# Kernel tuning notes

Measured on AMD Instinct MI355X. Metric: run time of the kernel, lower is better.

The kernel has to match this reference:

```python
import jax, jax.numpy as jnp
import numpy as np

NUM_HEADS = 16

def setup_inputs() -> dict:
    key = jax.random.key(0)
    ks = jax.random.split(key, 10)
    B, S, D = 2, 2048, 1024
    q = jax.random.normal(ks[0], (B, S, D), dtype=jnp.float32)
    k = jax.random.normal(ks[1], (B, S, D), dtype=jnp.float32)
    v = jax.random.normal(ks[2], (B, S, D), dtype=jnp.float32)
    mask = jax.random.randint(ks[3], (B, S), 0, 2, dtype=jnp.int32)
    scale = 0.02
    Wq = jax.random.normal(ks[4], (D, D), dtype=jnp.float32) * scale
    bq = jax.random.normal(ks[5], (D,), dtype=jnp.float32) * scale
    Wk = jax.random.normal(ks[6], (D, D), dtype=jnp.float32) * scale
    bk = jax.random.normal(ks[7], (D,), dtype=jnp.float32) * scale
    Wv = jax.random.normal(ks[8], (D, D), dtype=jnp.float32) * scale
    bv = jax.random.normal(ks[9], (D,), dtype=jnp.float32) * scale
    return {"q": q, "k": k, "v": v, "mask": mask,
            "Wq": Wq, "bq": bq, "Wk": Wk, "bk": bk, "Wv": Wv, "bv": bv}


def reference(q, k, v, mask, Wq, bq, Wk, bk, Wv, bv):
    B, S, D = q.shape
    H = NUM_HEADS
    dh = D // H
    # per-head split along last dim == reshape to (B, S, H, dh)
    Qh = (q @ Wq + bq).reshape(B, S, H, dh)
    Kh = (k @ Wk + bk).reshape(B, S, H, dh)
    Vh = (v @ Wv + bv).reshape(B, S, H, dh)
    # NOTE: original scales by sqrt(10), not sqrt(dim_per_head)
    scores = jnp.einsum('bqhd,bkhd->bhqk', Qh, Kh) / jnp.sqrt(jnp.float32(10.0))
    # mask [B,S] masks key positions; masked_fill replaces with -1e9
    scores = jnp.where(mask[:, None, None, :] == 0, jnp.float32(-1e9), scores)
    probs = jax.nn.softmax(scores, axis=-1)
    out = jnp.einsum('bhqk,bkhd->bqhd', probs, Vh).reshape(B, S, D)
    return out
```

## Files before the change

### kernel.cpp

```cpp
#include <hip/hip_runtime.h>
#include <hip/hip_bf16.h>

typedef __attribute__((ext_vector_type(8))) short short8;
typedef __attribute__((ext_vector_type(4))) float f32x4;

#define SC_L2E 0.4561727848849353f

#if __has_builtin(__builtin_amdgcn_exp2f)
#define EXP2F __builtin_amdgcn_exp2f
#else
#define EXP2F exp2f
#endif

static __device__ __forceinline__ void gload16(const void* g, void* l) {
  __builtin_amdgcn_global_load_lds((const __attribute__((address_space(1))) void*)g,
                                   (__attribute__((address_space(3))) void*)l, 16, 0, 0);
}

__global__ void k_cvt(const float* __restrict__ q, const float* __restrict__ kk,
                      const float* __restrict__ v, __hip_bfloat16* __restrict__ xb,
                      const float* __restrict__ Wq, const float* __restrict__ Wk,
                      const float* __restrict__ Wv, __hip_bfloat16* __restrict__ wt,
                      const int* __restrict__ mask, float* __restrict__ bias2) {
  __shared__ float T[64][65];
  if (blockIdx.x < 6144) {
    const size_t i = ((size_t)blockIdx.x * 256 + threadIdx.x) * 8;
    const int t = (int)(i >> 22);
    const float* src = (t == 0) ? q : (t == 1) ? kk : v;
    const size_t off = i & 4194303u;
    float4 f0 = *(const float4*)(src + off);
    float4 f1 = *(const float4*)(src + off + 4);
    union { short8 s; __hip_bfloat16 h[8]; } u;
    u.h[0] = __float2bfloat16(f0.x); u.h[1] = __float2bfloat16(f0.y);
    u.h[2] = __float2bfloat16(f0.z); u.h[3] = __float2bfloat16(f0.w);
    u.h[4] = __float2bfloat16(f1.x); u.h[5] = __float2bfloat16(f1.y);
    u.h[6] = __float2bfloat16(f1.z); u.h[7] = __float2bfloat16(f1.w);
    *(short8*)((char*)xb + i * 2) = u.s;
    return;
  }
  const int idx2 = blockIdx.x - 6144;
  const int z = idx2 >> 8;
  const int r2 = idx2 & 255;
  const int bxi = r2 & 15, byi = r2 >> 4;
  if (z == 0 && byi == 0) {
    const int idx = bxi * 256 + threadIdx.x;
    bias2[idx] = mask[idx] ? -12.0f : -1e30f;
  }
  const float* W = (z == 0) ? Wq : (z == 1) ? Wk : Wv;
  __hip_bfloat16* Wd = wt + (size_t)z * 1048576;
  const int n0 = bxi * 64, k0 = byi * 64;
  const int tx = threadIdx.x & 63, ty = threadIdx.x >> 6;
#pragma unroll
  for (int r = 0; r < 16; ++r)
    T[ty + r * 4][tx] = W[(size_t)(k0 + ty + r * 4) * 1024 + n0 + tx];
  __syncthreads();
#pragma unroll
  for (int r = 0; r < 16; ++r)
    Wd[(size_t)(n0 + ty + r * 4) * 1024 + k0 + tx] = __float2bfloat16(T[tx][ty + r * 4]);
}

__global__ __launch_bounds__(256) void k_proj(
    const __hip_bfloat16* __restrict__ xb, const __hip_bfloat16* __restrict__ wt,
    const float* __restrict__ bq, const float* __restrict__ bk, const float* __restrict__ bv,
    __hip_bfloat16* __restrict__ Qb, __hip_bfloat16* __restrict__ Kb,
    __hip_bfloat16* __restrict__ Vt) {
  __shared__ char smem[32768];
  char* As = smem;
  char* Bs = smem + 16384;
  const int orig = blockIdx.x;
  const int xcd = orig & 7, idx = orig >> 3;
  const int by = xcd * 4 + (idx & 3);
  const int bx = (idx >> 2) & 7;
  const int t = idx >> 5;
  const char* X = (const char*)(xb + (size_t)t * 4194304);
  const char* W = (const char*)(wt + (size_t)t * 1048576);
  const float* bias = (t == 0) ? bq : (t == 1) ? bk : bv;
  const int m0 = by * 128, n0 = bx * 128;
  const int tid = threadIdx.x, w = tid >> 6, lane = tid & 63;
  const int l15 = lane & 15, g = lane >> 4;
  const int l8 = lane >> 3, l7 = lane & 7;
  const int vswz = ((l7 ^ l8) << 4);
  const int wm = (w >> 1) * 64, wn = (w & 1) * 64;
  f32x4 acc[4][4];
#pragma unroll
  for (int i = 0; i < 4; ++i)
#pragma unroll
    for (int j = 0; j < 4; ++j) acc[i][j] = (f32x4){0.f, 0.f, 0.f, 0.f};

  for (int k0 = 0; k0 < 2048; k0 += 128) {
    __syncthreads();
#pragma unroll
    for (int j = 0; j < 4; ++j) {
      const int ch = w * 4 + j;
      gload16(X + (size_t)(m0 + ch * 8 + l8) * 2048 + k0 + vswz, As + ch * 1024);
      gload16(W + (size_t)(n0 + ch * 8 + l8) * 2048 + k0 + vswz, Bs + ch * 1024);
    }
    __syncthreads();
#pragma unroll
    for (int kk = 0; kk < 2; ++kk) {
      short8 af[4], bf_[4];
#pragma unroll
      for (int mt = 0; mt < 4; ++mt) {
        const int row = wm + mt * 16 + l15;
        af[mt] = *(const short8*)(As + row * 128 + ((kk * 64 + g * 16) ^ ((row & 7) << 4)));
      }
#pragma unroll
      for (int nt = 0; nt < 4; ++nt) {
        const int row = wn + nt * 16 + l15;
        bf_[nt] = *(const short8*)(Bs + row * 128 + ((kk * 64 + g * 16) ^ ((row & 7) << 4)));
      }
#pragma unroll
      for (int mt = 0; mt < 4; ++mt)
#pragma unroll
        for (int nt = 0; nt < 4; ++nt)
          acc[mt][nt] = __builtin_amdgcn_mfma_f32_16x16x32_bf16(af[mt], bf_[nt], acc[mt][nt], 0, 0, 0);
    }
  }

  float bv4[4];
#pragma unroll
  for (int nt = 0; nt < 4; ++nt) bv4[nt] = bias[n0 + wn + nt * 16 + l15];

  if (t < 2) {
#pragma unroll
    for (int mt = 0; mt < 4; ++mt) {
#pragma unroll
      for (int nt = 0; nt < 4; ++nt) {
        const int feat = n0 + wn + nt * 16 + l15;
        const int h = feat >> 6, d = feat & 63;
#pragma unroll
        for (int r = 0; r < 4; ++r) {
          const int token = m0 + wm + mt * 16 + g * 4 + r;
          const int b = token >> 11, s = token & 2047;
          const float val = acc[mt][nt][r] + bv4[nt];
          const __hip_bfloat16 hb = __float2bfloat16(val);
          if (t == 0) Qb[((size_t)(b * 16 + h) * 2048 + s) * 64 + d] = hb;
          else        Kb[((size_t)(b * 16 + h) * 2048 + s) * 64 + d] = hb;
        }
      }
    }
  } else {
    __hip_bfloat16* T2 = (__hip_bfloat16*)smem;
    const int bb = m0 >> 11;
    const int s0 = m0 & 2047;
#pragma unroll
    for (int p = 0; p < 2; ++p) {
      __syncthreads();
      if ((w >> 1) == p) {
#pragma unroll
        for (int mt = 0; mt < 4; ++mt)
#pragma unroll
          for (int nt = 0; nt < 4; ++nt) {
            const int feat = wn + nt * 16 + l15;
#pragma unroll
            for (int r = 0; r < 4; ++r) {
              const int tok = mt * 16 + g * 4 + r;
              T2[feat * 64 + (tok ^ ((feat & 7) << 3))] =
                  __float2bfloat16(acc[mt][nt][r] + bv4[nt]);
            }
          }
      }
      __syncthreads();
#pragma unroll
      for (int sw = 0; sw < 4; ++sw) {
        const int row = sw * 32 + (tid >> 3);
        const int c = tid & 7;
        const short8 vchunk = *(const short8*)(smem + row * 128 + 16 * (c ^ (row & 7)));
        const int gfeat = n0 + row;
        const int hh = gfeat >> 6, dd = gfeat & 63;
        *(short8*)(Vt + ((size_t)((bb * 16 + hh) * 64 + dd)) * 2048 + s0 + p * 64 + c * 8) = vchunk;
      }
    }
  }
}

#define ATTN_BODY(CUR, PRF, PREF)                                              \
  {                                                                            \
    float4 mb[4];                                                              \
    _Pragma("unroll") for (int nt = 0; nt < 4; ++nt)                           \
        mb[nt] = *(const float4*)(mbp + (nt >> 1) * 32 + ((nt & 1) << 2) + g * 8); \
    mbp += 64;                                                                 \
    if (PREF) {                                                                \
      gload16(kst, Ks[PRF] + w * 1024);                                        \
      gload16(vst, Vs[PRF] + w * 1024);                                        \
    }                                                                          \
    kst += 8192; vst += 128;                                                   \
    f32x4 s_[4];                                                               \
    __builtin_amdgcn_s_setprio(1);                                             \
    _Pragma("unroll") for (int nt = 0; nt < 4; ++nt) {                         \
      s_[nt] = (f32x4){0.f, 0.f, 0.f, 0.f};                                    \
      const int key = nt * 16 + l15;                                           \
      _Pragma("unroll") for (int kc = 0; kc < 2; ++kc) {                       \
        const short8 kf = *(const short8*)(Ks[CUR] + key * 128 +               \
                           ((kc * 64 + g * 16) ^ ((key & 7) << 4)));           \
        s_[nt] = __builtin_amdgcn_mfma_f32_16x16x32_bf16(kf, aq[kc], s_[nt], 0, 0, 0); \
      }                                                                        \
    }                                                                          \
    __builtin_amdgcn_s_setprio(0);                                             \
    short8 pb8[2];                                                             \
    _Pragma("unroll") for (int c = 0; c < 2; ++c) {                            \
      union { short8 s8; __hip_bfloat16 hh[8]; } pu;                           \
      pu.hh[0] = __float2bfloat16(EXP2F(fmaf(s_[2*c][0], SC_L2E, mb[2*c].x))); \
      pu.hh[1] = __float2bfloat16(EXP2F(fmaf(s_[2*c][1], SC_L2E, mb[2*c].y))); \
      pu.hh[2] = __float2bfloat16(EXP2F(fmaf(s_[2*c][2], SC_L2E, mb[2*c].z))); \
      pu.hh[3] = __float2bfloat16(EXP2F(fmaf(s_[2*c][3], SC_L2E, mb[2*c].w))); \
      pu.hh[4] = __float2bfloat16(EXP2F(fmaf(s_[2*c+1][0], SC_L2E, mb[2*c+1].x))); \
      pu.hh[5] = __float2bfloat16(EXP2F(fmaf(s_[2*c+1][1], SC_L2E, mb[2*c+1].y))); \
      pu.hh[6] = __float2bfloat16(EXP2F(fmaf(s_[2*c+1][2], SC_L2E, mb[2*c+1].z))); \
      pu.hh[7] = __float2bfloat16(EXP2F(fmaf(s_[2*c+1][3], SC_L2E, mb[2*c+1].w))); \
      pb8[c] = pu.s8;                                                          \
    }                                                                          \
    __builtin_amdgcn_s_setprio(1);                                             \
    lacc = __builtin_amdgcn_mfma_f32_16x16x32_bf16(ones8, pb8[0], lacc, 0, 0, 0); \
    lacc = __builtin_amdgcn_mfma_f32_16x16x32_bf16(ones8, pb8[1], lacc, 0, 0, 0); \
    _Pragma("unroll") for (int dt = 0; dt < 4; ++dt) {                         \
      const int d = dt * 16 + l15;                                             \
      const int sw2 = (d & 7) << 4;                                            \
      f32x4 o = oaccT[dt];                                                     \
      const short8 v0 = *(const short8*)(Vs[CUR] + d * 128 + ((g * 16) ^ sw2)); \
      const short8 v1 = *(const short8*)(Vs[CUR] + d * 128 + ((64 + g * 16) ^ sw2)); \
      o = __builtin_amdgcn_mfma_f32_16x16x32_bf16(v0, pb8[0], o, 0, 0, 0);     \
      o = __builtin_amdgcn_mfma_f32_16x16x32_bf16(v1, pb8[1], o, 0, 0, 0);     \
      oaccT[dt] = o;                                                           \
    }                                                                          \
    __builtin_amdgcn_s_setprio(0);                                             \
    asm volatile("s_waitcnt vmcnt(2)" ::: "memory");                           \
    __builtin_amdgcn_s_barrier();                                              \
    __builtin_amdgcn_sched_barrier(0);                                         \
  }

__global__ __launch_bounds__(512, 2) void k_attn(
    const __hip_bfloat16* __restrict__ Qb, const __hip_bfloat16* __restrict__ Kb,
    const __hip_bfloat16* __restrict__ Vt, const float* __restrict__ bias2,
    float* __restrict__ out) {
  __shared__ char Ks[3][8192];
  __shared__ char Vs[3][8192];
  const int orig = blockIdx.x;
  const int swz = (orig & 7) * 64 + (orig >> 3);
  const int bh = swz >> 4, qb = swz & 15;
  const int b = bh >> 4, h = bh & 15;
  const int tid = threadIdx.x, w = tid >> 6, lane = tid & 63;
  const int g = lane >> 4, l15 = lane & 15;
  const char* Qc = (const char*)(Qb + (size_t)bh * 131072);
  const char* Kc = (const char*)(Kb + (size_t)bh * 131072);
  const char* Vc = (const char*)(Vt + (size_t)bh * 131072);

  const int l8 = lane >> 3, l7 = lane & 7;
  const int vswz = ((l7 ^ l8) << 4);

  short8 aq[2];
  const int arow = qb * 128 + w * 16 + l15;
#pragma unroll
  for (int kc = 0; kc < 2; ++kc)
    aq[kc] = *(const short8*)(Qc + (size_t)arow * 128 + kc * 64 + g * 16);

  f32x4 oaccT[4];
#pragma unroll
  for (int i = 0; i < 4; ++i) oaccT[i] = (f32x4){0.f, 0.f, 0.f, 0.f};
  f32x4 lacc = (f32x4){0.f, 0.f, 0.f, 0.f};
  const short8 ones8 = {(short)0x3F80, (short)0x3F80, (short)0x3F80, (short)0x3F80,
                        (short)0x3F80, (short)0x3F80, (short)0x3F80, (short)0x3F80};

  const int s = w * 8 + l8;
  const int nt0 = s >> 4, gg = (s >> 2) & 3, rr = s & 3;
  const int kap = (nt0 >> 1) * 32 + gg * 8 + ((nt0 & 1) << 2) + rr;
  const char* kst = Kc + (size_t)kap * 128 + vswz;
  const char* vst = Vc + (size_t)s * 4096 + vswz;
  gload16(kst, Ks[0] + w * 1024);
  gload16(vst, Vs[0] + w * 1024);
  kst += 8192; vst += 128;
  gload16(kst, Ks[1] + w * 1024);
  gload16(vst, Vs[1] + w * 1024);
  kst += 8192; vst += 128;
  asm volatile("s_waitcnt vmcnt(2)" ::: "memory");
  __builtin_amdgcn_s_barrier();
  __builtin_amdgcn_sched_barrier(0);

  const float* mbp = bias2 + b * 2048;
  for (int kt = 0; kt < 30; kt += 3) {
    ATTN_BODY(0, 2, true)
    ATTN_BODY(1, 0, true)
    ATTN_BODY(2, 1, true)
  }
  ATTN_BODY(0, 2, false)
  ATTN_BODY(1, 0, false)

  const float rl = 1.0f / lacc[0];
  float* orow = out + ((size_t)(b * 2048 + arow)) * 1024 + h * 64;
#pragma unroll
  for (int dt = 0; dt < 4; ++dt) {
    float4 st;
    st.x = oaccT[dt][0] * rl; st.y = oaccT[dt][1] * rl;
    st.z = oaccT[dt][2] * rl; st.w = oaccT[dt][3] * rl;
    *(float4*)(orow + dt * 16 + g * 4) = st;
  }
}

extern "C" void kernel_launch(void* const* d_in, const int* in_sizes, int n_in,
                              void* d_out, int out_size, void* d_ws, size_t ws_size,
                              hipStream_t stream) {
  const float* q   = (const float*)d_in[0];
  const float* k   = (const float*)d_in[1];
  const float* v   = (const float*)d_in[2];
  const int* mask  = (const int*)d_in[3];
  const float* Wq  = (const float*)d_in[4];
  const float* bq  = (const float*)d_in[5];
  const float* Wk  = (const float*)d_in[6];
  const float* bk  = (const float*)d_in[7];
  const float* Wv  = (const float*)d_in[8];
  const float* bv  = (const float*)d_in[9];
  float* out = (float*)d_out;
  char* ws = (char*)d_ws;
  __hip_bfloat16* Xb = (__hip_bfloat16*)(ws);
  __hip_bfloat16* Wt = (__hip_bfloat16*)(ws + 25165824);
  __hip_bfloat16* Qb = (__hip_bfloat16*)(ws + 31457280);
  __hip_bfloat16* Kb = (__hip_bfloat16*)(ws + 39845888);
  __hip_bfloat16* Vt = (__hip_bfloat16*)(ws + 48234496);
  float* bias2      = (float*)(ws + 56623104);

  k_cvt<<<dim3(6912), dim3(256), 0, stream>>>(q, k, v, Xb, Wq, Wk, Wv, Wt, mask, bias2);
  k_proj<<<dim3(768), dim3(256), 0, stream>>>(Xb, Wt, bq, bk, bv, Qb, Kb, Vt);
  k_attn<<<dim3(512), dim3(512), 0, stream>>>(Qb, Kb, Vt, bias2, out);
}
```

Measured before the change: 103.9 us.

## Software-pipeline QK^T one tile ahead with four-stage K/V LDS ring

Restructures the attention loop so each iteration computes the QK^T scores for the next key tile while doing exp/PV for the current one, using ping-pong score registers. The LDS ring grows from three to four K/V buffers so loads are issued three tiles ahead, and the tail iterations are peeled with adjusted waitcnt and barrier handling. The aim is to hide the dependency between the score MFMAs and the exp/PV phase and to cover more global-load latency. In exchange it uses more LDS (64KB per block) and more registers, which may limit the two-blocks-per-CU occupancy.

```diff
diff --git a/kernel.cpp b/kernel.cpp
--- a/kernel.cpp
+++ b/kernel.cpp
@@ -174,40 +174,42 @@
   }
 }
 
-#define ATTN_BODY(CUR, PRF, PREF)                                              \
+#define ATTN_BODY(CUR, NXT, PRF, SP, SN, DOQK, DOPREF, SYNC)                   \
   {                                                                            \
     float4 mb[4];                                                              \
     _Pragma("unroll") for (int nt = 0; nt < 4; ++nt)                           \
         mb[nt] = *(const float4*)(mbp + (nt >> 1) * 32 + ((nt & 1) << 2) + g * 8); \
     mbp += 64;                                                                 \
-    if (PREF) {                                                                \
+    __builtin_amdgcn_sched_barrier(0);       \
+    if (DOPREF) {                                                              \
       gload16(kst, Ks[PRF] + w * 1024);                                        \
       gload16(vst, Vs[PRF] + w * 1024);                                        \
     }                                                                          \
     kst += 8192; vst += 128;                                                   \
-    f32x4 s_[4];                                                               \
-    __builtin_amdgcn_s_setprio(1);                                             \
-    _Pragma("unroll") for (int nt = 0; nt < 4; ++nt) {                         \
-      s_[nt] = (f32x4){0.f, 0.f, 0.f, 0.f};                                    \
-      const int key = nt * 16 + l15;                                           \
-      _Pragma("unroll") for (int kc = 0; kc < 2; ++kc) {                       \
-        const short8 kf = *(const short8*)(Ks[CUR] + key * 128 +               \
-                           ((kc * 64 + g * 16) ^ ((key & 7) << 4)));           \
-        s_[nt] = __builtin_amdgcn_mfma_f32_16x16x32_bf16(kf, aq[kc], s_[nt], 0, 0, 0); \
+    if (DOQK) {                                                                \
+      __builtin_amdgcn_s_setprio(1);                                           \
+      _Pragma("unroll") for (int nt = 0; nt < 4; ++nt) {                       \
+        SN[nt] = (f32x4){0.f, 0.f, 0.f, 0.f};                                  \
+        const int key = nt * 16 + l15;                                         \
+        _Pragma("unroll") for (int kc = 0; kc < 2; ++kc) {                     \
+          const short8 kf = *(const short8*)(Ks[NXT] + key * 128 +             \
+                             ((kc * 64 + g * 16) ^ ((key & 7) << 4)));         \
+          SN[nt] = __builtin_amdgcn_mfma_f32_16x16x32_bf16(kf, aq[kc], SN[nt], 0, 0, 0); \
+        }                                                                      \
       }                                                                        \
-    }                                                                          \
-    __builtin_amdgcn_s_setprio(0);                                             \
+      __builtin_amdgcn_s_setprio(0);                                           \
+    }                                                                          \
     short8 pb8[2];                                                             \
     _Pragma("unroll") for (int c = 0; c < 2; ++c) {                            \
       union { short8 s8; __hip_bfloat16 hh[8]; } pu;                           \
-      pu.hh[0] = __float2bfloat16(EXP2F(fmaf(s_[2*c][0], SC_L2E, mb[2*c].x))); \
-      pu.hh[1] = __float2bfloat16(EXP2F(fmaf(s_[2*c][1], SC_L2E, mb[2*c].y))); \
-      pu.hh[2] = __float2bfloat16(EXP2F(fmaf(s_[2*c][2], SC_L2E, mb[2*c].z))); \
-      pu.hh[3] = __float2bfloat16(EXP2F(fmaf(s_[2*c][3], SC_L2E, mb[2*c].w))); \
-      pu.hh[4] = __float2bfloat16(EXP2F(fmaf(s_[2*c+1][0], SC_L2E, mb[2*c+1].x))); \
-      pu.hh[5] = __float2bfloat16(EXP2F(fmaf(s_[2*c+1][1], SC_L2E, mb[2*c+1].y))); \
-      pu.hh[6] = __float2bfloat16(EXP2F(fmaf(s_[2*c+1][2], SC_L2E, mb[2*c+1].z))); \
-      pu.hh[7] = __float2bfloat16(EXP2F(fmaf(s_[2*c+1][3], SC_L2E, mb[2*c+1].w))); \
+      pu.hh[0] = __float2bfloat16(EXP2F(fmaf(SP[2*c][0], SC_L2E, mb[2*c].x))); \
+      pu.hh[1] = __float2bfloat16(EXP2F(fmaf(SP[2*c][1], SC_L2E, mb[2*c].y))); \
+      pu.hh[2] = __float2bfloat16(EXP2F(fmaf(SP[2*c][2], SC_L2E, mb[2*c].z))); \
+      pu.hh[3] = __float2bfloat16(EXP2F(fmaf(SP[2*c][3], SC_L2E, mb[2*c].w))); \
+      pu.hh[4] = __float2bfloat16(EXP2F(fmaf(SP[2*c+1][0], SC_L2E, mb[2*c+1].x))); \
+      pu.hh[5] = __float2bfloat16(EXP2F(fmaf(SP[2*c+1][1], SC_L2E, mb[2*c+1].y))); \
+      pu.hh[6] = __float2bfloat16(EXP2F(fmaf(SP[2*c+1][2], SC_L2E, mb[2*c+1].z))); \
+      pu.hh[7] = __float2bfloat16(EXP2F(fmaf(SP[2*c+1][3], SC_L2E, mb[2*c+1].w))); \
       pb8[c] = pu.s8;                                                          \
     }                                                                          \
     __builtin_amdgcn_s_setprio(1);                                             \
@@ -224,17 +226,20 @@
       oaccT[dt] = o;                                                           \
     }                                                                          \
     __builtin_amdgcn_s_setprio(0);                                             \
-    asm volatile("s_waitcnt vmcnt(2)" ::: "memory");                           \
-    __builtin_amdgcn_s_barrier();                                              \
-    __builtin_amdgcn_sched_barrier(0);                                         \
+    if (SYNC == 2) { asm volatile("s_waitcnt vmcnt(2)" ::: "memory"); }        \
+    else if (SYNC == 0) { asm volatile("s_waitcnt vmcnt(0)" ::: "memory"); }   \
+    if (SYNC >= 0) {                                                           \
+      __builtin_amdgcn_s_barrier();                                            \
+      __builtin_amdgcn_sched_barrier(0);                                       \
+    }                                                                          \
   }
 
 __global__ __launch_bounds__(512, 2) void k_attn(
     const __hip_bfloat16* __restrict__ Qb, const __hip_bfloat16* __restrict__ Kb,
     const __hip_bfloat16* __restrict__ Vt, const float* __restrict__ bias2,
     float* __restrict__ out) {
-  __shared__ char Ks[3][8192];
-  __shared__ char Vs[3][8192];
+  __shared__ char Ks[4][8192];
+  __shared__ char Vs[4][8192];
   const int orig = blockIdx.x;
   const int swz = (orig & 7) * 64 + (orig >> 3);
   const int bh = swz >> 4, qb = swz & 15;
@@ -260,30 +265,48 @@
   f32x4 lacc = (f32x4){0.f, 0.f, 0.f, 0.f};
   const short8 ones8 = {(short)0x3F80, (short)0x3F80, (short)0x3F80, (short)0x3F80,
                         (short)0x3F80, (short)0x3F80, (short)0x3F80, (short)0x3F80};
-
-  const int s = w * 8 + l8;
-  const int nt0 = s >> 4, gg = (s >> 2) & 3, rr = s & 3;
+  f32x4 sA[4], sB[4];
+
+  const int slot = w * 8 + l8;
+  const int nt0 = slot >> 4, gg = (slot >> 2) & 3, rr = slot & 3;
   const int kap = (nt0 >> 1) * 32 + gg * 8 + ((nt0 & 1) << 2) + rr;
   const char* kst = Kc + (size_t)kap * 128 + vswz;
-  const char* vst = Vc + (size_t)s * 4096 + vswz;
-  gload16(kst, Ks[0] + w * 1024);
-  gload16(vst, Vs[0] + w * 1024);
-  kst += 8192; vst += 128;
-  gload16(kst, Ks[1] + w * 1024);
-  gload16(vst, Vs[1] + w * 1024);
-  kst += 8192; vst += 128;
+  const char* vst = Vc + (size_t)slot * 4096 + vswz;
+#pragma unroll
+  for (int tpre = 0; tpre < 3; ++tpre) {
+    gload16(kst, Ks[tpre] + w * 1024);
+    gload16(vst, Vs[tpre] + w * 1024);
+    kst += 8192; vst += 128;
+  }
   asm volatile("s_waitcnt vmcnt(2)" ::: "memory");
   __builtin_amdgcn_s_barrier();
   __builtin_amdgcn_sched_barrier(0);
 
+  __builtin_amdgcn_s_setprio(1);
+#pragma unroll
+  for (int nt = 0; nt < 4; ++nt) {
+    sA[nt] = (f32x4){0.f, 0.f, 0.f, 0.f};
+    const int key = nt * 16 + l15;
+#pragma unroll
+    for (int kc = 0; kc < 2; ++kc) {
+      const short8 kf = *(const short8*)(Ks[0] + key * 128 +
+                         ((kc * 64 + g * 16) ^ ((key & 7) << 4)));
+      sA[nt] = __builtin_amdgcn_mfma_f32_16x16x32_bf16(kf, aq[kc], sA[nt], 0, 0, 0);
+    }
+  }
+  __builtin_amdgcn_s_setprio(0);
+
   const float* mbp = bias2 + b * 2048;
-  for (int kt = 0; kt < 30; kt += 3) {
-    ATTN_BODY(0, 2, true)
-    ATTN_BODY(1, 0, true)
-    ATTN_BODY(2, 1, true)
-  }
-  ATTN_BODY(0, 2, false)
-  ATTN_BODY(1, 0, false)
+  for (int k = 0; k < 7; ++k) {
+    ATTN_BODY(0, 1, 3, sA, sB, 1, 1, 2)
+    ATTN_BODY(1, 2, 0, sB, sA, 1, 1, 2)
+    ATTN_BODY(2, 3, 1, sA, sB, 1, 1, 2)
+    ATTN_BODY(3, 0, 2, sB, sA, 1, 1, 2)
+  }
+  ATTN_BODY(0, 1, 3, sA, sB, 1, 1, 2)
+  ATTN_BODY(1, 2, 0, sB, sA, 1, 0, 0)
+  ATTN_BODY(2, 3, 1, sA, sB, 1, 0, 0)
+  ATTN_BODY(3, 0, 2, sB, sA, 0, 0, -1)
 
   const float rl = 1.0f / lacc[0];
   float* orow = out + ((size_t)(b * 2048 + arow)) * 1024 + h * 64;
```

Result: no change. 103.8 us (-0.1%).
